# Optimization experiments

Measured on AMD Instinct MI355X. Metric: run time of the kernel, lower is better.

Reference implementation:

```python
import jax, jax.numpy as jnp
import numpy as np
from jax import lax

EPS = 1e-5

def _bn_train(x, gamma, beta):
    # BatchNorm2d in training mode: batch stats over (N,H,W), biased variance
    mean = jnp.mean(x, axis=(0, 2, 3), keepdims=True)
    var = jnp.mean((x - mean) ** 2, axis=(0, 2, 3), keepdims=True)
    xhat = (x - mean) * lax.rsqrt(var + EPS)
    return gamma[None, :, None, None] * xhat + beta[None, :, None, None]

def _binact(x):
    # forward: sign(x); backward (STE): identity where |x|<=1, zero elsewhere
    y = jnp.where(jnp.abs(x) > 1.0, lax.stop_gradient(x), x)
    return y + lax.stop_gradient(jnp.sign(y) - y)

def _binconv(x, w, padding):
    # per-output-channel alpha = mean(|w|) over (in,kh,kw); w_bin = sign(w)*alpha with STE
    alpha = jnp.mean(jnp.abs(w), axis=(1, 2, 3), keepdims=True)
    w_bin = lax.stop_gradient(jnp.sign(w) * alpha - w) + w
    return lax.conv_general_dilated(
        x, w_bin, window_strides=(1, 1),
        padding=[(padding, padding), (padding, padding)],
        dimension_numbers=("NCHW", "OIHW", "NCHW"))

def setup_inputs() -> dict:
    key = jax.random.key(0)
    ks = jax.random.split(key, 10)
    B, Cin, Cout, H, W, T = 32, 128, 256, 64, 64, 512
    x = jax.random.normal(ks[0], (B, Cin, H, W), jnp.float32)
    t = jax.random.normal(ks[1], (B, T), jnp.float32)
    # conv weights, kaiming-ish scale
    w1 = jax.random.normal(ks[2], (Cout, Cin, 3, 3), jnp.float32) * (1.0 / np.sqrt(Cin * 9))
    w2 = jax.random.normal(ks[3], (Cout, Cout, 3, 3), jnp.float32) * (1.0 / np.sqrt(Cout * 9))
    wskip = jax.random.normal(ks[4], (Cout, Cin, 1, 1), jnp.float32) * (1.0 / np.sqrt(Cin))
    gamma1 = 1.0 + 0.1 * jax.random.normal(ks[5], (Cin,), jnp.float32)
    beta1 = 0.1 * jax.random.normal(ks[6], (Cin,), jnp.float32)
    gamma2 = 1.0 + 0.1 * jax.random.normal(ks[7], (Cout,), jnp.float32)
    beta2 = 0.1 * jax.random.normal(ks[8], (Cout,), jnp.float32)
    tw = jax.random.normal(ks[9], (Cout, T), jnp.float32) * (1.0 / np.sqrt(T))
    tb = jnp.zeros((Cout,), jnp.float32)
    return {"x": x, "t": t, "w1": w1, "w2": w2, "wskip": wskip,
            "gamma1": gamma1, "beta1": beta1, "gamma2": gamma2, "beta2": beta2,
            "tw": tw, "tb": tb}

def reference(x, t, w1, w2, wskip, gamma1, beta1, gamma2, beta2, tw, tb):
    h = _binconv(_binact(_bn_train(x, gamma1, beta1)), w1, padding=1)
    temb = t @ tw.T + tb                      # [B, Cout]
    h = h + temb[:, :, None, None]
    h = _binconv(_binact(_bn_train(h, gamma2, beta2)), w2, padding=1)
    return h + _binconv(x, wskip, padding=0)
```

## Files before the change

kernel.cpp:

```cpp
#include <hip/hip_runtime.h>
#include <stdint.h>

typedef unsigned short u16;
typedef uint8_t u8;
typedef __attribute__((ext_vector_type(8))) short short8;
typedef __attribute__((ext_vector_type(4))) float f32x4;
typedef __attribute__((ext_vector_type(4))) int i32x4;

#define EPSF 1e-5f
#define LGKM0 asm volatile("s_waitcnt lgkmcnt(0)" ::: "memory")
#define VM0   asm volatile("s_waitcnt vmcnt(0)" ::: "memory")
#define VM2   asm volatile("s_waitcnt vmcnt(2)" ::: "memory")
#define BAR   __builtin_amdgcn_s_barrier()
#define GLL(src, dst) __builtin_amdgcn_global_load_lds(                     \
    (const __attribute__((address_space(1))) void*)(src),                   \
    (__attribute__((address_space(3))) void*)(dst), 16, 0, 0)

__device__ __forceinline__ u16 f2bf(float f) {
  uint32_t u = __float_as_uint(f);
  u += 0x7FFFu + ((u >> 16) & 1u);
  return (u16)(u >> 16);
}
__device__ __forceinline__ u8 sgn8(float y) {
  return y > 0.f ? (u8)1 : (y < 0.f ? (u8)0xFF : (u8)0);
}

__global__ void bn1_stage1(const float* __restrict__ x, float* __restrict__ p1) {
  int c = blockIdx.x >> 2, s = blockIdx.x & 3;
  int tid = threadIdx.x;
  float sum = 0.f, sq = 0.f;
  for (int n = s * 8; n < s * 8 + 8; ++n) {
    const f32x4* bp = (const f32x4*)(x + (((size_t)(n * 128 + c)) << 12));
    #pragma unroll 4
    for (int i = tid; i < 1024; i += 256) {
      f32x4 v = bp[i];
      sum += v[0] + v[1] + v[2] + v[3];
      sq  += v[0]*v[0] + v[1]*v[1] + v[2]*v[2] + v[3]*v[3];
    }
  }
  __shared__ float rs[256], rq[256];
  rs[tid] = sum; rq[tid] = sq; __syncthreads();
  for (int st = 128; st > 0; st >>= 1) {
    if (tid < st) { rs[tid] += rs[tid + st]; rq[tid] += rq[tid + st]; }
    __syncthreads();
  }
  if (tid == 0) { p1[blockIdx.x] = rs[0]; p1[512 + blockIdx.x] = rq[0]; }
}

__global__ void bn1_stage2(const float* __restrict__ p1, const float* __restrict__ g,
                           const float* __restrict__ b, float* __restrict__ sc,
                           float* __restrict__ off) {
  int c = threadIdx.x;
  float s = 0.f, q = 0.f;
  for (int k = 0; k < 4; ++k) { s += p1[c * 4 + k]; q += p1[512 + c * 4 + k]; }
  float mean = s * (1.f / 131072.f);
  float var  = q * (1.f / 131072.f) - mean * mean;
  float is = rsqrtf(var + EPSF);
  float scv = g[c] * is;
  sc[c] = scv;
  off[c] = b[c] - mean * scv;
}

__global__ void bn2_stage2b(const float* __restrict__ pS, const float* __restrict__ pQ,
                            const float* __restrict__ g, const float* __restrict__ bb,
                            float* __restrict__ sc, float* __restrict__ off) {
  int o = blockIdx.x, t = threadIdx.x;
  __shared__ float rs[256], rq[256];
  float s = 0.f, q = 0.f;
  #pragma unroll
  for (int k = 0; k < 8; ++k) {
    size_t j = t + k * 256;
    s += pS[j * 256 + o];
    q += pQ[j * 256 + o];
  }
  rs[t] = s; rq[t] = q; __syncthreads();
  for (int st = 128; st > 0; st >>= 1) {
    if (t < st) { rs[t] += rs[t + st]; rq[t] += rq[t + st]; }
    __syncthreads();
  }
  if (t == 0) {
    float mean = rs[0] * (1.f / 131072.f);
    float var  = rq[0] * (1.f / 131072.f) - mean * mean;
    float is = rsqrtf(var + EPSF);
    float scv = g[o] * is;
    sc[o] = scv;
    off[o] = bb[o] - mean * scv;
  }
}

__device__ __forceinline__ float blk_reduce(float v, float* red) {
  int t = threadIdx.x;
  red[t] = v; __syncthreads();
  for (int st = 128; st > 0; st >>= 1) {
    if (t < st) red[t] += red[t + st];
    __syncthreads();
  }
  float r = red[0]; __syncthreads();
  return r;
}

__global__ void prep_weights(const float* __restrict__ w1, const float* __restrict__ w2,
                             const float* __restrict__ wsk, u8* __restrict__ w1s,
                             u8* __restrict__ w2s, u16* __restrict__ wskr,
                             float* __restrict__ alpha1, float* __restrict__ alpha2) {
  int o = blockIdx.x, t = threadIdx.x;
  int rg8 = o >> 5, ol = o & 31;
  __shared__ float red[256];
  float s = 0.f;
  for (int j = t; j < 1152; j += 256) s += fabsf(w1[(size_t)o * 1152 + j]);
  float a1 = blk_reduce(s, red) * (1.f / 1152.f);
  if (t == 0) alpha1[o] = a1;
  for (int j = t; j < 1152; j += 256) {
    int st = j >> 6, k = j & 63;
    int cc = st / 9, tap = st % 9;
    int ch = cc * 64 + k;
    size_t idx = (size_t)(st * 8 + rg8) * 2048 +
                 ((ol << 2) + ((k >> 4) ^ ((ol >> 1) & 3))) * 16 + (k & 15);
    w1s[idx] = sgn8(w1[(size_t)o * 1152 + ch * 9 + tap]);
  }
  s = 0.f;
  for (int j = t; j < 2304; j += 256) s += fabsf(w2[(size_t)o * 2304 + j]);
  float a2 = blk_reduce(s, red) * (1.f / 2304.f);
  if (t == 0) alpha2[o] = a2;
  for (int j = t; j < 2304; j += 256) {
    int st = j >> 6, k = j & 63;
    int c4 = st / 9, tap = st % 9;
    int ch = c4 * 64 + k;
    size_t idx = (size_t)(st * 8 + rg8) * 2048 +
                 ((ol << 2) + ((k >> 4) ^ ((ol >> 1) & 3))) * 16 + (k & 15);
    w2s[idx] = sgn8(w2[(size_t)o * 2304 + ch * 9 + tap]);
  }
  s = 0.f;
  for (int j = t; j < 128; j += 256) s += fabsf(wsk[o * 128 + j]);
  float ask = blk_reduce(s, red) * (1.f / 128.f);
  float ratio = ask / a2;
  int nf = (o >> 4) & 1, li = o & 15;
  for (int j = t; j < 128; j += 256) {
    int e = j >> 6, c = j & 63;
    int ks = c >> 5, kq = (c >> 3) & 3, jj = c & 7;
    float w = wsk[o * 128 + j];
    float v = w > 0.f ? ratio : (w < 0.f ? -ratio : 0.f);
    wskr[((size_t)((e * 8 + rg8) * 64 + kq * 16 + li)) * 32 + (ks * 2 + nf) * 8 + jj] =
        f2bf(v);
  }
}

__global__ void temb_k(const float* __restrict__ t, const float* __restrict__ tw,
                       const float* __restrict__ tb, float* __restrict__ temb) {
  int bb = blockIdx.x, o = threadIdx.x;
  __shared__ float tl[512];
  tl[o] = t[bb * 512 + o];
  tl[o + 256] = t[bb * 512 + 256 + o];
  __syncthreads();
  float acc = tb[o];
  #pragma unroll 8
  for (int k = 0; k < 512; ++k) acc += tl[k] * tw[(size_t)o * 512 + k];
  temb[bb * 256 + o] = acc;
}

__global__ void border_zero(u8* __restrict__ Abuf) {
  u8* plane = Abuf + (size_t)blockIdx.x * 278784;
  int tid = threadIdx.x;
  i32x4 z = {};
  for (int idx = tid; idx < 260; idx += 256) {
    int row, px;
    if (idx < 66) { row = 0; px = idx; }
    else if (idx < 132) { row = 65; px = idx - 66; }
    else { int e = idx - 132; row = 1 + (e >> 1); px = (e & 1) * 65; }
    u8* p = plane + (size_t)(row * 66 + px) * 64;
    #pragma unroll
    for (int i = 0; i < 4; ++i) *(i32x4*)(p + i * 16) = z;
  }
}

__global__ void binact1(const float* __restrict__ x, const float* __restrict__ sc,
                        const float* __restrict__ off, u8* __restrict__ a1p,
                        u16* __restrict__ xb) {
  int b = blockIdx.x >> 6, y = blockIdx.x & 63, tid = threadIdx.x;
  __shared__ u8  ls[64 * 144];
  __shared__ u16 lx[64 * 136];
  int c = tid >> 1, x0 = (tid & 1) * 32;
  const float* src = x + (((size_t)(b * 128 + c)) << 12) + y * 64 + x0;
  float s0 = sc[c], o0 = off[c];
  #pragma unroll
  for (int i = 0; i < 32; i += 4) {
    f32x4 v = *(const f32x4*)(src + i);
    #pragma unroll
    for (int j = 0; j < 4; ++j) {
      int xc = x0 + i + j;
      float yv = s0 * v[j] + o0;
      ls[xc * 144 + c] = sgn8(yv);
      lx[xc * 136 + c] = f2bf(v[j]);
    }
  }
  __syncthreads();
  int xx = tid >> 2, cg = (tid & 3) * 32;
  int cc = cg >> 6, ch0 = cg & 63;
  u8*  pdst = a1p + ((size_t)(b * 2 + cc) * 4356 + (y + 1) * 66 + xx + 1) * 64 + ch0;
  u16* xdst = xb + ((size_t)blockIdx.x * 64 + xx) * 128 + cg;
  *(i32x4*)(pdst)      = *(const i32x4*)&ls[xx * 144 + cg];
  *(i32x4*)(pdst + 16) = *(const i32x4*)&ls[xx * 144 + cg + 16];
  #pragma unroll
  for (int i = 0; i < 32; i += 8)
    *(i32x4*)(xdst + i) = *(const i32x4*)&lx[xx * 136 + cg + i];
}

__global__ void binact2(const float* __restrict__ h, const float* __restrict__ sc,
                        const float* __restrict__ off, u8* __restrict__ a2p) {
  int b = blockIdx.x >> 6, y = blockIdx.x & 63, tid = threadIdx.x;
  __shared__ float s_sc[256], s_off[256];
  s_sc[tid] = sc[tid]; s_off[tid] = off[tid];
  __syncthreads();
  const f32x4* src = (const f32x4*)(h + (size_t)blockIdx.x * 16384);
  #pragma unroll 4
  for (int i = tid; i < 4096; i += 256) {
    f32x4 v = src[i];
    int px = i >> 6, c0 = (i & 63) * 4;
    int c4 = c0 >> 6, chm = c0 & 63;
    uint32_t p = (uint32_t)sgn8(s_sc[c0 + 0] * v[0] + s_off[c0 + 0]) |
                 ((uint32_t)sgn8(s_sc[c0 + 1] * v[1] + s_off[c0 + 1]) << 8) |
                 ((uint32_t)sgn8(s_sc[c0 + 2] * v[2] + s_off[c0 + 2]) << 16) |
                 ((uint32_t)sgn8(s_sc[c0 + 3] * v[3] + s_off[c0 + 3]) << 24);
    u8* dst = a2p + ((size_t)(b * 4 + c4) * 4356 + (y + 1) * 66 + px + 1) * 64 + chm;
    *(uint32_t*)dst = p;
  }
}

template <int NCHUNK, bool SKIP, bool ADD_TEMB, bool STATS, bool DIRECT>
__global__ __launch_bounds__(512, 2) void convk(
    const u8* __restrict__ Apl, const u16* __restrict__ xb,
    const u8* __restrict__ wS, const u16* __restrict__ wskr,
    const float* __restrict__ alpha, const float* __restrict__ temb,
    float* __restrict__ outp, float* __restrict__ pS, float* __restrict__ pQ) {
  constexpr int NS = NCHUNK * 9;
  __shared__ u8 smem[45440];
  u8* lA = smem;
  u8* lB = smem + 12672;
  const int tid = threadIdx.x;
  const int lane = tid & 63, wn = tid >> 6;
  const int kq = lane >> 4, li = lane & 15;

  const int bid = blockIdx.x;
  const int tile = (bid & 7) * 256 + (bid >> 3);
  const int m0 = tile * 64;
  const int b = tile >> 6, y = tile & 63;

  auto issueB = [&](int s) {
    const u8* src = wS + (size_t)s * 16384 + wn * 2048 + lane * 16;
    u8* dst = lB + (s & 1) * 16384 + wn * 2048;
    GLL(src, dst);
    GLL(src + 1024, dst + 1024);
  };

  auto winLoad = [&](int c) {
    const u8* gp = Apl + (size_t)(b * NCHUNK + c) * 278784 + (size_t)y * 4224;
    {
      int g = tid;
      int row = g / 264, rem = g - row * 264;
      int px = rem >> 2, sl = rem & 3;
      const u8* src = gp + (size_t)(row * 66 + px) * 64 + ((sl ^ ((px >> 1) & 3)) << 4);
      u8* dst = lA + (size_t)(tid & ~63) * 16;
      GLL(src, dst);
    }
    if (tid < 280) {
      int g = 512 + tid;
      int row = g / 264, rem = g - row * 264;
      int px = rem >> 2, sl = rem & 3;
      const u8* src = gp + (size_t)(row * 66 + px) * 64 + ((sl ^ ((px >> 1) & 3)) << 4);
      u8* dst = lA + (size_t)((512 + (tid & ~63)) & ~63) * 16;
      GLL(src, dst);
    }
  };

  const u8* pA[3];
  #pragma unroll
  for (int dx = 0; dx < 3; ++dx)
    pA[dx] = lA + (li + dx) * 64 + ((kq ^ (((li + dx) >> 1) & 3)) << 4);
  const u8* pB = lB + wn * 2048 + li * 64 + ((kq ^ ((li >> 1) & 3)) << 4);

  i32x4 acc[4][2] = {};

  auto compute = [&](int tap, int buf) {
    const int dy = tap / 3, dx = tap % 3;
    i32x4 av[4], bv[2];
    #pragma unroll
    for (int f = 0; f < 4; ++f)
      av[f] = *(const i32x4*)(pA[dx] + dy * 4224 + f * 1024);
    #pragma unroll
    for (int nf = 0; nf < 2; ++nf)
      bv[nf] = *(const i32x4*)(pB + buf * 16384 + nf * 1024);
    __builtin_amdgcn_s_setprio(1);
    #pragma unroll
    for (int mf = 0; mf < 4; ++mf)
      #pragma unroll
      for (int nf = 0; nf < 2; ++nf)
        acc[mf][nf] = __builtin_amdgcn_mfma_i32_16x16x64_i8(
            av[mf], bv[nf], acc[mf][nf], 0, 0, 0);
    __builtin_amdgcn_s_setprio(0);
  };

  winLoad(0);
  issueB(0);
  issueB(1);
  VM0;
  BAR;

  #pragma unroll
  for (int s = 0; s < NS; ++s) {
    if (NCHUNK > 1 && s > 0 && (s % 9) == 0) {
      LGKM0; BAR;
      winLoad(s / 9);
      VM0; BAR;
    }
    if (s + 2 < NS) { VM2; } else { VM0; }
    compute(s % 9, s & 1);
    LGKM0;
    if (s + 2 < NS) issueB(s + 2);
  }

  f32x4 facc[4][2];
  if constexpr (SKIP) {
    #pragma unroll
    for (int mf = 0; mf < 4; ++mf)
      #pragma unroll
      for (int nf = 0; nf < 2; ++nf)
        #pragma unroll
        for (int r = 0; r < 4; ++r)
          facc[mf][nf][r] = (float)acc[mf][nf][r];
    const u8* pAs[2];
    #pragma unroll
    for (int ks = 0; ks < 2; ++ks)
      pAs[ks] = lA + li * 128 + ((((ks << 2) + kq) ^ (li & 7)) << 4);
    LGKM0; BAR;
    #pragma unroll
    for (int e = 0; e < 2; ++e) {
      {
        int g = tid;
        int m = g >> 3, sl = g & 7;
        const u8* src = (const u8*)xb + (size_t)(m0 + m) * 256 + e * 128 +
                        ((sl ^ (m & 7)) << 4);
        u8* dst = lA + (size_t)(tid & ~63) * 16;
        GLL(src, dst);
      }
      const u16* bbase = wskr + ((size_t)((e * 8 + wn) * 64) + lane) * 32;
      short8 sb[4];
      #pragma unroll
      for (int i = 0; i < 4; ++i) sb[i] = *(const short8*)(bbase + i * 8);
      VM0; BAR;
      #pragma unroll
      for (int ks = 0; ks < 2; ++ks) {
        short8 av[4];
        #pragma unroll
        for (int f = 0; f < 4; ++f) av[f] = *(const short8*)(pAs[ks] + f * 2048);
        __builtin_amdgcn_s_setprio(1);
        #pragma unroll
        for (int mf = 0; mf < 4; ++mf)
          #pragma unroll
          for (int nf = 0; nf < 2; ++nf)
            facc[mf][nf] = __builtin_amdgcn_mfma_f32_16x16x32_bf16(
                av[mf], sb[ks * 2 + nf], facc[mf][nf], 0, 0, 0);
        __builtin_amdgcn_s_setprio(0);
      }
      if (e == 0) { LGKM0; BAR; }
    }
  }

  const int cb = wn * 32 + li;

  if constexpr (STATS) {
    float als[2], tas[2];
    #pragma unroll
    for (int nf = 0; nf < 2; ++nf) {
      int o = cb + nf * 16;
      als[nf] = alpha[o];
      tas[nf] = ADD_TEMB ? temb[b * 256 + o] : 0.f;
    }
    float ps[2] = {0.f, 0.f}, pq[2] = {0.f, 0.f};
    #pragma unroll
    for (int nf = 0; nf < 2; ++nf)
      #pragma unroll
      for (int mf = 0; mf < 4; ++mf)
        #pragma unroll
        for (int r = 0; r < 4; ++r) {
          float v = (float)acc[mf][nf][r] * als[nf] + tas[nf];
          ps[nf] += v; pq[nf] += v * v;
        }
    #pragma unroll
    for (int nf = 0; nf < 2; ++nf) {
      ps[nf] += __shfl_xor(ps[nf], 16); ps[nf] += __shfl_xor(ps[nf], 32);
      pq[nf] += __shfl_xor(pq[nf], 16); pq[nf] += __shfl_xor(pq[nf], 32);
    }
    if (lane < 16) {
      #pragma unroll
      for (int nf = 0; nf < 2; ++nf) {
        pS[(size_t)bid * 256 + wn * 32 + nf * 16 + lane] = ps[nf];
        pQ[(size_t)bid * 256 + wn * 32 + nf * 16 + lane] = pq[nf];
      }
    }
    __syncthreads();
    float* ld = (float*)smem;
    const int c3 = li & 3;
    #pragma unroll
    for (int p = 0; p < 4; ++p) {
      #pragma unroll
      for (int nf = 0; nf < 2; ++nf) {
        int colg0 = (cb >> 2) + nf * 4;
        #pragma unroll
        for (int r = 0; r < 4; ++r) {
          int rloc = 4 * kq + r;
          float v = (float)acc[p][nf][r] * als[nf] + tas[nf];
          ld[rloc * 256 + ((colg0 ^ kq) << 2) + c3] = v;
        }
      }
      __syncthreads();
      #pragma unroll
      for (int it = 0; it < 2; ++it) {
        int flat = tid + it * 512;
        int row = flat >> 6, c4 = flat & 63;
        int c4p = c4 ^ ((row >> 2) & 3);
        f32x4 v = *(const f32x4*)&ld[row * 256 + c4p * 4];
        *(f32x4*)(outp + (size_t)(m0 + p * 16 + row) * 256 + c4 * 4) = v;
      }
      __syncthreads();
    }
  } else if constexpr (DIRECT) {
    float* tb2 = (float*)smem;
    float* obase = outp + (((size_t)(b * 256)) << 12) + (m0 & 4095);
    __syncthreads();
    #pragma unroll
    for (int c4 = 0; c4 < 4; ++c4) {
      if ((wn >> 1) == c4) {
        #pragma unroll
        for (int nf = 0; nf < 2; ++nf) {
          int cq = (wn & 1) * 32 + nf * 16 + li;
          float al = alpha[c4 * 64 + cq];
          #pragma unroll
          for (int mf = 0; mf < 4; ++mf) {
            int cs = cq ^ ((mf >> 1) & 3);
            #pragma unroll
            for (int r = 0; r < 4; ++r)
              tb2[(mf * 16 + 4 * kq + r) * 65 + cs] = facc[mf][nf][r] * al;
          }
        }
      }
      __syncthreads();
      #pragma unroll
      for (int it = 0; it < 2; ++it) {
        int flat = tid + it * 512;
        int ch = flat >> 4, mg = flat & 15;
        int chs = ch ^ ((mg >> 3) & 3);
        f32x4 v;
        #pragma unroll
        for (int e = 0; e < 4; ++e) v[e] = tb2[(mg * 4 + e) * 65 + chs];
        *(f32x4*)(obase + (((size_t)(c4 * 64 + ch)) << 12) + mg * 4) = v;
      }
      __syncthreads();
    }
  }
}

extern "C" void kernel_launch(void* const* d_in, const int* in_sizes, int n_in,
                              void* d_out, int out_size, void* d_ws, size_t ws_size,
                              hipStream_t stream) {
  const float* x      = (const float*)d_in[0];
  const float* t      = (const float*)d_in[1];
  const float* w1     = (const float*)d_in[2];
  const float* w2     = (const float*)d_in[3];
  const float* wskip  = (const float*)d_in[4];
  const float* gamma1 = (const float*)d_in[5];
  const float* beta1  = (const float*)d_in[6];
  const float* gamma2 = (const float*)d_in[7];
  const float* beta2  = (const float*)d_in[8];
  const float* tw     = (const float*)d_in[9];
  const float* tb     = (const float*)d_in[10];
  float* out = (float*)d_out;

  uint8_t* base = (uint8_t*)d_ws;
  size_t off = 0;
  auto alloc = [&](size_t bytes) {
    void* p = base + off;
    off += (bytes + 255) & ~(size_t)255;
    return p;
  };
  u8* Abuf     = (u8*)alloc((size_t)192 * 278784);
  u8* a1p      = Abuf;
  u8* a2p      = Abuf + (size_t)64 * 278784;
  u16* xb      = (u16*)alloc((size_t)131072 * 128 * 2);
  float* h     = (float*)alloc((size_t)131072 * 256 * 4);
  u8* w1s      = (u8*)alloc((size_t)18 * 16384);
  u8* w2s      = (u8*)alloc((size_t)36 * 16384);
  u16* wskr    = (u16*)alloc((size_t)2 * 8 * 4096);
  float* temb  = (float*)alloc(32 * 256 * 4);
  float* alpha1 = (float*)alloc(256 * 4);
  float* alpha2 = (float*)alloc(256 * 4);
  float* p1    = (float*)alloc(1024 * 4);
  float* pS    = (float*)alloc((size_t)2048 * 256 * 4);
  float* pQ    = (float*)alloc((size_t)2048 * 256 * 4);
  float* sc1   = (float*)alloc(128 * 4);
  float* off1  = (float*)alloc(128 * 4);
  float* sc2   = (float*)alloc(256 * 4);
  float* off2  = (float*)alloc(256 * 4);

  border_zero<<<192, 256, 0, stream>>>(Abuf);

  bn1_stage1<<<512, 256, 0, stream>>>(x, p1);
  bn1_stage2<<<1, 128, 0, stream>>>(p1, gamma1, beta1, sc1, off1);
  prep_weights<<<256, 256, 0, stream>>>(w1, w2, wskip, w1s, w2s, wskr, alpha1, alpha2);
  temb_k<<<32, 256, 0, stream>>>(t, tw, tb, temb);
  binact1<<<2048, 256, 0, stream>>>(x, sc1, off1, a1p, xb);

  convk<2, false, true, true, false><<<2048, 512, 0, stream>>>(
      a1p, xb, w1s, (const u16*)nullptr, alpha1, temb, h, pS, pQ);

  bn2_stage2b<<<256, 256, 0, stream>>>(pS, pQ, gamma2, beta2, sc2, off2);
  binact2<<<2048, 256, 0, stream>>>(h, sc2, off2, a2p);

  convk<4, true, false, false, true><<<2048, 512, 0, stream>>>(
      a2p, xb, w2s, wskr, alpha2, (const float*)nullptr, out,
      (float*)nullptr, (float*)nullptr);

  (void)in_sizes; (void)n_in; (void)out_size; (void)ws_size;
}
```

Baseline: 290.0 us.

## Load conv weight fragments directly into registers instead of staging through LDS

The binarized weight operand for the int8 MFMA conv is now read straight from global memory into per-lane registers, double-buffered across taps, rather than copied into LDS with global_load_lds and read back. The weight prep kernel changes its packing so each lane's two 16-byte fragments are contiguous. This removes LDS traffic for B and cuts LDS use from about 45KB to about 17KB, which may allow more blocks per CU. In exchange, weight reads now come from global/L2 on every tap with compiler-managed waits, and register pressure rises.

Measured after the change: 282.5 us. 2.6% less time.

```diff
diff --git a/kernel.cpp b/kernel.cpp
--- a/kernel.cpp
+++ b/kernel.cpp
@@ -10,7 +10,6 @@
 #define EPSF 1e-5f
 #define LGKM0 asm volatile("s_waitcnt lgkmcnt(0)" ::: "memory")
 #define VM0   asm volatile("s_waitcnt vmcnt(0)" ::: "memory")
-#define VM2   asm volatile("s_waitcnt vmcnt(2)" ::: "memory")
 #define BAR   __builtin_amdgcn_s_barrier()
 #define GLL(src, dst) __builtin_amdgcn_global_load_lds(                     \
     (const __attribute__((address_space(1))) void*)(src),                   \
@@ -104,7 +103,7 @@
                              u8* __restrict__ w2s, u16* __restrict__ wskr,
                              float* __restrict__ alpha1, float* __restrict__ alpha2) {
   int o = blockIdx.x, t = threadIdx.x;
-  int rg8 = o >> 5, ol = o & 31;
+  int rg8 = o >> 5;
   __shared__ float red[256];
   float s = 0.f;
   for (int j = t; j < 1152; j += 256) s += fabsf(w1[(size_t)o * 1152 + j]);
@@ -114,8 +113,8 @@
     int st = j >> 6, k = j & 63;
     int cc = st / 9, tap = st % 9;
     int ch = cc * 64 + k;
-    size_t idx = (size_t)(st * 8 + rg8) * 2048 +
-                 ((ol << 2) + ((k >> 4) ^ ((ol >> 1) & 3))) * 16 + (k & 15);
+    size_t idx = ((size_t)((st * 8 + rg8) * 64 + (k >> 4) * 16 + (o & 15))) * 32 +
+                 ((o >> 4) & 1) * 16 + (k & 15);
     w1s[idx] = sgn8(w1[(size_t)o * 1152 + ch * 9 + tap]);
   }
   s = 0.f;
@@ -126,8 +125,8 @@
     int st = j >> 6, k = j & 63;
     int c4 = st / 9, tap = st % 9;
     int ch = c4 * 64 + k;
-    size_t idx = (size_t)(st * 8 + rg8) * 2048 +
-                 ((ol << 2) + ((k >> 4) ^ ((ol >> 1) & 3))) * 16 + (k & 15);
+    size_t idx = ((size_t)((st * 8 + rg8) * 64 + (k >> 4) * 16 + (o & 15))) * 32 +
+                 ((o >> 4) & 1) * 16 + (k & 15);
     w2s[idx] = sgn8(w2[(size_t)o * 2304 + ch * 9 + tap]);
   }
   s = 0.f;
@@ -229,13 +228,12 @@
 template <int NCHUNK, bool SKIP, bool ADD_TEMB, bool STATS, bool DIRECT>
 __global__ __launch_bounds__(512, 2) void convk(
     const u8* __restrict__ Apl, const u16* __restrict__ xb,
-    const u8* __restrict__ wS, const u16* __restrict__ wskr,
+    const u8* __restrict__ wB, const u16* __restrict__ wskr,
     const float* __restrict__ alpha, const float* __restrict__ temb,
     float* __restrict__ outp, float* __restrict__ pS, float* __restrict__ pQ) {
   constexpr int NS = NCHUNK * 9;
-  __shared__ u8 smem[45440];
+  __shared__ u8 smem[16896];
   u8* lA = smem;
-  u8* lB = smem + 12672;
   const int tid = threadIdx.x;
   const int lane = tid & 63, wn = tid >> 6;
   const int kq = lane >> 4, li = lane & 15;
@@ -245,11 +243,11 @@
   const int m0 = tile * 64;
   const int b = tile >> 6, y = tile & 63;
 
-  auto issueB = [&](int s) {
-    const u8* src = wS + (size_t)s * 16384 + wn * 2048 + lane * 16;
-    u8* dst = lB + (s & 1) * 16384 + wn * 2048;
-    GLL(src, dst);
-    GLL(src + 1024, dst + 1024);
+  const u8* wlane = wB + (size_t)wn * 2048 + (size_t)lane * 32;
+  auto loadB = [&](int s, i32x4 (&dst)[2]) {
+    const u8* src = wlane + (size_t)s * 16384;
+    dst[0] = *(const i32x4*)src;
+    dst[1] = *(const i32x4*)(src + 16);
   };
 
   auto winLoad = [&](int c) {
@@ -267,7 +265,7 @@
       int row = g / 264, rem = g - row * 264;
       int px = rem >> 2, sl = rem & 3;
       const u8* src = gp + (size_t)(row * 66 + px) * 64 + ((sl ^ ((px >> 1) & 3)) << 4);
-      u8* dst = lA + (size_t)((512 + (tid & ~63)) & ~63) * 16;
+      u8* dst = lA + (size_t)(512 + (tid & ~63)) * 16;
       GLL(src, dst);
     }
   };
@@ -276,32 +274,29 @@
   #pragma unroll
   for (int dx = 0; dx < 3; ++dx)
     pA[dx] = lA + (li + dx) * 64 + ((kq ^ (((li + dx) >> 1) & 3)) << 4);
-  const u8* pB = lB + wn * 2048 + li * 64 + ((kq ^ ((li >> 1) & 3)) << 4);
 
   i32x4 acc[4][2] = {};
 
-  auto compute = [&](int tap, int buf) {
+  auto compute = [&](int tap, i32x4 (&bcur)[2]) {
     const int dy = tap / 3, dx = tap % 3;
-    i32x4 av[4], bv[2];
+    i32x4 av[4];
     #pragma unroll
     for (int f = 0; f < 4; ++f)
       av[f] = *(const i32x4*)(pA[dx] + dy * 4224 + f * 1024);
-    #pragma unroll
-    for (int nf = 0; nf < 2; ++nf)
-      bv[nf] = *(const i32x4*)(pB + buf * 16384 + nf * 1024);
     __builtin_amdgcn_s_setprio(1);
     #pragma unroll
     for (int mf = 0; mf < 4; ++mf)
       #pragma unroll
       for (int nf = 0; nf < 2; ++nf)
         acc[mf][nf] = __builtin_amdgcn_mfma_i32_16x16x64_i8(
-            av[mf], bv[nf], acc[mf][nf], 0, 0, 0);
+            av[mf], bcur[nf], acc[mf][nf], 0, 0, 0);
     __builtin_amdgcn_s_setprio(0);
   };
 
   winLoad(0);
-  issueB(0);
-  issueB(1);
+  i32x4 bA[2], bB[2];
+  loadB(0, bA);
+  loadB(1, bB);
   VM0;
   BAR;
 
@@ -312,10 +307,13 @@
       winLoad(s / 9);
       VM0; BAR;
     }
-    if (s + 2 < NS) { VM2; } else { VM0; }
-    compute(s % 9, s & 1);
-    LGKM0;
-    if (s + 2 < NS) issueB(s + 2);
+    if ((s & 1) == 0) {
+      compute(s % 9, bA);
+      if (s + 2 < NS) loadB(s + 2, bA);
+    } else {
+      compute(s % 9, bB);
+      if (s + 2 < NS) loadB(s + 2, bB);
+    }
   }
 
   f32x4 facc[4][2];
```
